# Kernel optimization log

Hardware: AMD Instinct MI355X
Metric: run time of the kernel (lower is better)

The kernel has to match this reference:

```python
import jax, jax.numpy as jnp
import numpy as np

B, N, F, H, OUT, K, L = 32, 2048, 3, 64, 128, 16, 3


def _edge_mlp(e, w1, b1, wo, bo):
    # Faithful to the given MLP.forward: layer1 -> ReLU -> output (layer2 is skipped!)
    return jax.nn.relu(e @ w1 + b1) @ wo + bo


def _dynamic_edge_conv(x, k, w1, b1, wo, bo):
    # x: [B, N, D]. kNN in feature space (self included, distance 0), per graph.
    sq = jnp.sum(x * x, axis=-1)                                   # [B, N]
    d2 = sq[:, :, None] + sq[:, None, :] - 2.0 * jnp.einsum('bnd,bmd->bnm', x, x)
    _, idx = jax.lax.top_k(-d2, k)                                 # [B, N, K]
    x_j = jax.vmap(lambda xb, ib: xb[ib])(x, idx)                  # [B, N, K, D] gather
    x_i = jnp.broadcast_to(x[:, :, None, :], x_j.shape)
    e = jnp.concatenate([x_i, x_j - x_i], axis=-1)                 # EdgeConv message [B,N,K,2D]
    h = _edge_mlp(e, w1, b1, wo, bo)                               # [B, N, K, H]
    return jnp.mean(h, axis=2)                                     # aggr='mean' -> [B, N, H]


def setup_inputs() -> dict:
    key = jax.random.key(0)
    ks = jax.random.split(key, 20)
    inp = {'x': jax.random.normal(ks[0], (B, N, F), dtype=jnp.float32)}
    kit = iter(ks[1:])
    for i in range(L):
        din = 2 * F if i == 0 else 2 * H
        inp[f'w1_{i}'] = jax.random.normal(next(kit), (din, H), jnp.float32) / np.sqrt(din)
        inp[f'b1_{i}'] = jnp.zeros((H,), jnp.float32)
        inp[f'wo_{i}'] = jax.random.normal(next(kit), (H, H), jnp.float32) / np.sqrt(H)
        inp[f'bo_{i}'] = jnp.zeros((H,), jnp.float32)
    inp['fw1'] = jax.random.normal(next(kit), (H, H), jnp.float32) / np.sqrt(H)
    inp['fb1'] = jnp.zeros((H,), jnp.float32)
    inp['fw2'] = jax.random.normal(next(kit), (H, OUT), jnp.float32) / np.sqrt(H)
    inp['fb2'] = jnp.zeros((OUT,), jnp.float32)
    return inp


def reference(x, w1_0, b1_0, wo_0, bo_0, w1_1, b1_1, wo_1, bo_1, w1_2, b1_2, wo_2, bo_2, fw1, fb1, fw2, fb2):
    layers = [(w1_0, b1_0, wo_0, bo_0), (w1_1, b1_1, wo_1, bo_1), (w1_2, b1_2, wo_2, bo_2)]
    h = x
    for (w1, b1, wo, bo) in layers:
        h = _dynamic_edge_conv(h, K, w1, b1, wo, bo)
    g = jnp.mean(h, axis=1)                                        # global_mean_pool -> [B, H]
    return jax.nn.relu(g @ fw1 + fb1) @ fw2 + fb2                  # [B, OUT]
```

## Files before the change

kernel.cpp:

```cpp
#include <hip/hip_runtime.h>

#define BB 32
#define NN 2048
#define FF 3
#define HH 64
#define OUTC 128
#define KK 16
#define BN (BB * NN)

typedef __attribute__((ext_vector_type(8))) __bf16 bf16x8;
typedef __attribute__((ext_vector_type(4))) float f32x4;

__device__ __forceinline__ unsigned int packkey(float d2, unsigned int m) {
    unsigned int bb = __builtin_bit_cast(unsigned int, d2);
    unsigned int msk = (unsigned int)((int)bb >> 31);
    unsigned int srt = bb ^ (msk | 0x80000000u);
    return (srt & 0xFFFFF800u) | m;
}

__device__ __forceinline__ unsigned long long pack64(float d2, unsigned int j) {
    unsigned int bb = __builtin_bit_cast(unsigned int, d2);
    unsigned int msk = (unsigned int)((int)bb >> 31);
    unsigned int srt = bb ^ (msk | 0x80000000u);
    return ((unsigned long long)srt << 11) | j;
}

__device__ __forceinline__ void ce(unsigned int& a, unsigned int& b) {
    unsigned int lo = a < b ? a : b;
    unsigned int hi = a < b ? b : a;
    a = lo; b = hi;
}

__device__ __forceinline__ void sort16(unsigned int k[16]) {
#pragma unroll
    for (int p = 1; p < 16; p <<= 1)
#pragma unroll
        for (int q = p; q >= 1; q >>= 1)
#pragma unroll
            for (int j = q % p; j + q < 16; j += 2 * q)
#pragma unroll
                for (int i = 0; i < q; ++i) {
                    int x = i + j, y = i + j + q;
                    if (y < 16 && (x / (2 * p) == y / (2 * p))) ce(k[x], k[y]);
                }
}

__device__ __forceinline__ void merge16(unsigned int keys[16], const unsigned int nk[16]) {
    unsigned int t[16];
#pragma unroll
    for (int i = 0; i < 16; ++i) {
        unsigned int b = nk[15 - i];
        t[i] = keys[i] < b ? keys[i] : b;
    }
#pragma unroll
    for (int d = 8; d >= 1; d >>= 1)
#pragma unroll
        for (int i = 0; i < 16; ++i)
            if ((i & d) == 0) ce(t[i], t[i ^ d]);
#pragma unroll
    for (int i = 0; i < 16; ++i) keys[i] = t[i];
}

__global__ __launch_bounds__(256) void prep3_kernel(const float* __restrict__ x,
                                                    const float* __restrict__ w1,
                                                    const float* __restrict__ b1,
                                                    float* __restrict__ sqo,
                                                    float* __restrict__ P,
                                                    float* __restrict__ Q) {
    const int tid = threadIdx.x;
    const int h = tid & 63;
    const int pl = tid >> 6;
    const long p = (long)blockIdx.x * 4 + pl;
    const float* fp = x + p * 3;
    const float f0 = fp[0], f1 = fp[1], f2 = fp[2];
    if (h == 0) sqo[p] = f0 * f0 + f1 * f1 + f2 * f2;
    float accp = 0.f, accq = 0.f;
    const float fv[3] = {f0, f1, f2};
#pragma unroll
    for (int d = 0; d < 3; ++d) {
        float wa = w1[d * HH + h];
        float wb = w1[(3 + d) * HH + h];
        accp = fmaf(fv[d], wa - wb, accp);
        accq = fmaf(fv[d], wb, accq);
    }
    P[p * HH + h] = accp + b1[h];
    Q[p * HH + h] = accq;
}

__global__ __launch_bounds__(256) void prep64_kernel(const float* __restrict__ feat,
                                                     const float* __restrict__ w1,
                                                     const float* __restrict__ b1,
                                                     __bf16* __restrict__ fbf,
                                                     float* __restrict__ sqo,
                                                     float* __restrict__ P,
                                                     float* __restrict__ Q) {
    __shared__ float rows[64 * HH];
    const int tid = threadIdx.x;
    const int h = tid & 63;
    const int wv = tid >> 6;
    const long row0 = (long)blockIdx.x * 64;

    float wdiff[64], wbv[64];
#pragma unroll
    for (int d = 0; d < 64; ++d) {
        float wa = w1[d * HH + h];
        float wb_ = w1[(HH + d) * HH + h];
        wdiff[d] = wa - wb_;
        wbv[d] = wb_;
    }
    const float bv = b1[h];

    {
        const float4* src = (const float4*)(feat + row0 * HH);
        float4* dst = (float4*)rows;
#pragma unroll
        for (int i = 0; i < 4; ++i) dst[tid + 256 * i] = src[tid + 256 * i];
    }
    __syncthreads();

    for (int r = wv * 16; r < wv * 16 + 16; ++r) {
        const long p = row0 + r;
        float fvh = rows[r * HH + h];
        fbf[p * HH + h] = (__bf16)fvh;
        float s = fvh * fvh;
        s += __shfl_xor(s, 1);
        s += __shfl_xor(s, 2);
        s += __shfl_xor(s, 4);
        s += __shfl_xor(s, 8);
        s += __shfl_xor(s, 16);
        s += __shfl_xor(s, 32);
        if (h == 0) sqo[p] = s;

        float ap0 = 0.f, ap1 = 0.f, aq0 = 0.f, aq1 = 0.f;
#pragma unroll
        for (int d4 = 0; d4 < 16; ++d4) {
            float4 fv = *(const float4*)&rows[r * HH + d4 * 4];
            ap0 = fmaf(fv.x, wdiff[4 * d4 + 0], ap0);
            aq0 = fmaf(fv.x, wbv[4 * d4 + 0], aq0);
            ap1 = fmaf(fv.y, wdiff[4 * d4 + 1], ap1);
            aq1 = fmaf(fv.y, wbv[4 * d4 + 1], aq1);
            ap0 = fmaf(fv.z, wdiff[4 * d4 + 2], ap0);
            aq0 = fmaf(fv.z, wbv[4 * d4 + 2], aq0);
            ap1 = fmaf(fv.w, wdiff[4 * d4 + 3], ap1);
            aq1 = fmaf(fv.w, wbv[4 * d4 + 3], aq1);
        }
        P[p * HH + h] = (ap0 + ap1) + bv;
        Q[p * HH + h] = aq0 + aq1;
    }
}

__global__ __launch_bounds__(256) void knn3_filter_kernel(const float* __restrict__ x,
                                                          const float* __restrict__ sq,
                                                          unsigned short* __restrict__ idx32) {
    __shared__ float4 lds_c[256];
    __shared__ unsigned int Km[64 * 68];
    const int tid = threadIdx.x;
    const int xcd = blockIdx.x & 7;
    const int ii = blockIdx.x >> 3;
    const int b = xcd + 8 * (ii >> 5);
    const int rg = ii & 31;
    const long pbase = (long)b * NN;
    const int r = tid >> 2, slot = tid & 3;
    const int row = rg * 64 + r;

    const float* rp = x + (pbase + row) * 3;
    const float xr0 = rp[0], xr1 = rp[1], xr2 = rp[2];

    unsigned int keys[KK];
#pragma unroll
    for (int j = 0; j < KK; ++j) keys[j] = 0xFFFFFFFFu;

    float c0, c1, c2, c3;
    {
        const float* cp = x + (pbase + tid) * 3;
        c0 = cp[0]; c1 = cp[1]; c2 = cp[2]; c3 = sq[pbase + tid];
    }

    for (int t = 0; t < NN / 256; ++t) {
        __syncthreads();
        lds_c[tid] = make_float4(c0, c1, c2, c3);
        __syncthreads();
        if (t < NN / 256 - 1) {
            const int m = (t + 1) * 256 + tid;
            const float* cp = x + (pbase + m) * 3;
            c0 = cp[0]; c1 = cp[1]; c2 = cp[2]; c3 = sq[pbase + m];
        }
#pragma unroll
        for (int bb = 0; bb < 4; ++bb) {
            unsigned int nk[16];
#pragma unroll
            for (int cc = 0; cc < 16; ++cc) {
                const int li = bb * 64 + cc * 4 + slot;
                float4 v = lds_c[li];
                float dot = fmaf(xr0, v.x, fmaf(xr1, v.y, xr2 * v.z));
                float d2 = fmaf(-2.0f, dot, v.w);
                nk[cc] = packkey(d2, (unsigned int)(t * 256 + li));
            }
            sort16(nk);
            merge16(keys, nk);
        }
    }

    {
        uint4* kw = (uint4*)&Km[r * 68 + slot * 16];
#pragma unroll
        for (int q = 0; q < 4; ++q)
            kw[q] = make_uint4(keys[4 * q], keys[4 * q + 1], keys[4 * q + 2], keys[4 * q + 3]);
    }
    __syncthreads();
    if (slot < 2) {
        const unsigned int* k0 = &Km[r * 68 + slot * 32];
        const unsigned int* k1 = k0 + 16;
        unsigned short ms[16];
#pragma unroll
        for (int j = 0; j < 16; ++j) {
            unsigned int a = k0[j], bv = k1[15 - j];
            ms[j] = (unsigned short)((a < bv ? a : bv) & 0x7FFu);
        }
        uint4* op = (uint4*)(idx32 + ((pbase + row) * 32 + slot * 16));
        op[0] = ((const uint4*)ms)[0];
        op[1] = ((const uint4*)ms)[1];
    }
}

#define APAD 72
#define DPAD 68

__global__ __launch_bounds__(256) void knn_filter_kernel(const __bf16* __restrict__ fbf,
                                                         const float* __restrict__ sq,
                                                         unsigned short* __restrict__ idx32) {
    __shared__ __align__(16) unsigned char smem[2 * 64 * APAD * 2];
    __shared__ __align__(16) float SqD[2 * 64];

    const int tid = threadIdx.x;
    const int xcd = blockIdx.x & 7;
    const int ii = blockIdx.x >> 3;
    const int b = xcd + 8 * (ii >> 5);
    const int rg = ii & 31;
    const long pbase = (long)b * NN;
    const int row0 = rg * 64;
    const int ci = tid >> 2, ch = tid & 3;
    const int wv = tid >> 6, ln = tid & 63;
    const int n16 = ln & 15, quad = ln >> 4;

    bf16x8 rf0, rf1;
    {
        const __bf16* rp = fbf + (pbase + row0 + wv * 16 + n16) * 64 + quad * 8;
        rf0 = *(const bf16x8*)rp;
        rf1 = *(const bf16x8*)(rp + 32);
    }

    unsigned int keys[KK];
#pragma unroll
    for (int j = 0; j < KK; ++j) keys[j] = 0xFFFFFFFFu;

    uint4 pv0, pv1;
    float psq;
    {
        const __bf16* src = fbf + (pbase + ci) * 64 + ch * 16;
        pv0 = *(const uint4*)src;
        pv1 = *(const uint4*)(src + 8);
        psq = (tid < 64) ? sq[pbase + tid] : 0.f;
    }
    {
        __bf16* B0 = (__bf16*)smem;
        *(uint4*)&B0[ci * APAD + ch * 16] = pv0;
        *(uint4*)&B0[ci * APAD + ch * 16 + 8] = pv1;
        if (tid < 64) SqD[tid] = psq;
    }
    __syncthreads();

    for (int t = 0; t < NN / 64; ++t) {
        const int cur = t & 1;
        const __bf16* Bc = (const __bf16*)smem + cur * 64 * APAD;
        const float* Sc = SqD + cur * 64;

        if (t < NN / 64 - 1) {
            const __bf16* src = fbf + (pbase + (long)(t + 1) * 64 + ci) * 64 + ch * 16;
            pv0 = *(const uint4*)src;
            pv1 = *(const uint4*)(src + 8);
            if (tid < 64) psq = sq[pbase + (t + 1) * 64 + tid];
        }

        unsigned int nk[16];
#pragma unroll
        for (int ct = 0; ct < 4; ++ct) {
            const __bf16* cp = &Bc[(ct * 16 + n16) * APAD + quad * 8];
            bf16x8 cf0 = *(const bf16x8*)cp;
            bf16x8 cf1 = *(const bf16x8*)(cp + 32);
            f32x4 acc = {0.f, 0.f, 0.f, 0.f};
            acc = __builtin_amdgcn_mfma_f32_16x16x32_bf16(cf0, rf0, acc, 0, 0, 0);
            acc = __builtin_amdgcn_mfma_f32_16x16x32_bf16(cf1, rf1, acc, 0, 0, 0);
            f32x4 sv = *(const f32x4*)&Sc[ct * 16 + quad * 4];
            const unsigned int mb = (unsigned int)(t * 64 + ct * 16 + quad * 4);
#pragma unroll
            for (int rr = 0; rr < 4; ++rr)
                nk[ct * 4 + rr] = packkey(fmaf(-2.0f, acc[rr], sv[rr]), mb + rr);
        }

        if (t < NN / 64 - 1) {
            __bf16* Bn = (__bf16*)smem + (cur ^ 1) * 64 * APAD;
            *(uint4*)&Bn[ci * APAD + ch * 16] = pv0;
            *(uint4*)&Bn[ci * APAD + ch * 16 + 8] = pv1;
            if (tid < 64) SqD[(cur ^ 1) * 64 + tid] = psq;
        }

        sort16(nk);
        merge16(keys, nk);

        __syncthreads();
    }

    unsigned int* stg = (unsigned int*)smem;
    {
        uint4* kw = (uint4*)&stg[(wv * 16 + n16) * DPAD + quad * 16];
#pragma unroll
        for (int q = 0; q < 4; ++q)
            kw[q] = make_uint4(keys[4 * q], keys[4 * q + 1], keys[4 * q + 2], keys[4 * q + 3]);
    }
    __syncthreads();
    const int r = tid >> 2, slot = tid & 3;
    if (slot < 2) {
        const unsigned int* k0 = &stg[r * DPAD + slot * 32];
        const unsigned int* k1 = k0 + 16;
        unsigned short ms[16];
#pragma unroll
        for (int j = 0; j < 16; ++j) {
            unsigned int a = k0[j], bv = k1[15 - j];
            ms[j] = (unsigned short)((a < bv ? a : bv) & 0x7FFu);
        }
        uint4* op = (uint4*)(idx32 + ((pbase + row0 + r) * 32 + slot * 16));
        op[0] = ((const uint4*)ms)[0];
        op[1] = ((const uint4*)ms)[1];
    }
}

template <int D>
__global__ __launch_bounds__(256) void rescore_gather_kernel(const float* __restrict__ feat,
                                                             const float* __restrict__ sq,
                                                             const unsigned short* __restrict__ idx32,
                                                             const float* __restrict__ P,
                                                             const float* __restrict__ Q,
                                                             const float* __restrict__ wo,
                                                             const float* __restrict__ bo,
                                                             float* __restrict__ outf) {
    __shared__ unsigned long long ScK[4][2][32];
    __shared__ int Li[4][2][KK];
    __shared__ float Rl[4][2][HH];

    const int tid = threadIdx.x;
    const int wv = tid >> 6, ln = tid & 63;
    const int rw = ln >> 5, c = ln & 31;
    const int xcd = blockIdx.x & 7;
    const int ii = blockIdx.x >> 3;
    const int batch = xcd + 8 * (ii >> 8);
    const int rb = ii & 255;
    const long pbase = (long)batch * NN;
    const long pblk = pbase + (long)rb * 8;
    const int rA = wv * 2;
    const long prow = pblk + rA + rw;

    const int jown = (int)idx32[prow * 32 + c];
    const float sqown = sq[pbase + jown];

    if constexpr (D == 64) {
        const int cg = ln >> 2, e = ln & 3;
#pragma unroll
        for (int rr = 0; rr < 2; ++rr) {
            const float* rbase = feat + (pblk + rA + rr) * 64;
            const float4 rv0 = *(const float4*)(rbase + 0 * 16 + e * 4);
            const float4 rv1 = *(const float4*)(rbase + 1 * 16 + e * 4);
            const float4 rv2 = *(const float4*)(rbase + 2 * 16 + e * 4);
            const float4 rv3 = *(const float4*)(rbase + 3 * 16 + e * 4);
#pragma unroll
            for (int pp = 0; pp < 2; ++pp) {
                const int srcl = rr * 32 + pp * 16 + cg;
                const int jq = __shfl(jown, srcl);
                const float sqc = __shfl(sqown, srcl);
                const float* cb = feat + (pbase + jq) * 64;
                const float4 cv0 = *(const float4*)(cb + 0 * 16 + e * 4);
                const float4 cv1 = *(const float4*)(cb + 1 * 16 + e * 4);
                const float4 cv2 = *(const float4*)(cb + 2 * 16 + e * 4);
                const float4 cv3 = *(const float4*)(cb + 3 * 16 + e * 4);
                float part = 0.f;
                part = fmaf(rv0.x, cv0.x, part); part = fmaf(rv0.y, cv0.y, part);
                part = fmaf(rv0.z, cv0.z, part); part = fmaf(rv0.w, cv0.w, part);
                part = fmaf(rv1.x, cv1.x, part); part = fmaf(rv1.y, cv1.y, part);
                part = fmaf(rv1.z, cv1.z, part); part = fmaf(rv1.w, cv1.w, part);
                part = fmaf(rv2.x, cv2.x, part); part = fmaf(rv2.y, cv2.y, part);
                part = fmaf(rv2.z, cv2.z, part); part = fmaf(rv2.w, cv2.w, part);
                part = fmaf(rv3.x, cv3.x, part); part = fmaf(rv3.y, cv3.y, part);
                part = fmaf(rv3.z, cv3.z, part); part = fmaf(rv3.w, cv3.w, part);
                part += __shfl_xor(part, 1);
                part += __shfl_xor(part, 2);
                if (e == 0)
                    ScK[wv][rr][pp * 16 + cg] =
                        pack64(fmaf(-2.0f, part, sqc), (unsigned int)jq);
            }
        }
    } else {
        const float* rp = feat + prow * 3;
        const float xr0 = rp[0], xr1 = rp[1], xr2 = rp[2];
        const float* cp = feat + (pbase + jown) * 3;
        const float dot = fmaf(xr0, cp[0], fmaf(xr1, cp[1], xr2 * cp[2]));
        ScK[wv][rw][c] = pack64(fmaf(-2.0f, dot, sqown), (unsigned int)jown);
    }
    asm volatile("s_waitcnt lgkmcnt(0)" ::: "memory");
    __builtin_amdgcn_sched_barrier(0);

    {
        const unsigned long long mykey = ScK[wv][rw][c];
        int rank = 0;
#pragma unroll
        for (int m = 0; m < 32; ++m)
            rank += (ScK[wv][rw][m] < mykey) ? 1 : 0;
        if (rank < KK) Li[wv][rw][rank] = (int)(mykey & 0x7FFu);
    }
    asm volatile("s_waitcnt lgkmcnt(0)" ::: "memory");
    __builtin_amdgcn_sched_barrier(0);

    const int h = ln;
    const long pA = pblk + rA;
    const float PvA = P[pA * HH + h];
    const float PvB = P[(pA + 1) * HH + h];
    float accA = 0.f, accB = 0.f;
#pragma unroll
    for (int kq = 0; kq < 4; ++kq) {
        const int4 a4 = *(const int4*)&Li[wv][0][kq * 4];
        const int4 b4 = *(const int4*)&Li[wv][1][kq * 4];
        accA += fmaxf(PvA + Q[(pbase + a4.x) * HH + h], 0.f);
        accA += fmaxf(PvA + Q[(pbase + a4.y) * HH + h], 0.f);
        accA += fmaxf(PvA + Q[(pbase + a4.z) * HH + h], 0.f);
        accA += fmaxf(PvA + Q[(pbase + a4.w) * HH + h], 0.f);
        accB += fmaxf(PvB + Q[(pbase + b4.x) * HH + h], 0.f);
        accB += fmaxf(PvB + Q[(pbase + b4.y) * HH + h], 0.f);
        accB += fmaxf(PvB + Q[(pbase + b4.z) * HH + h], 0.f);
        accB += fmaxf(PvB + Q[(pbase + b4.w) * HH + h], 0.f);
    }
    Rl[wv][0][h] = accA * (1.f / KK);
    Rl[wv][1][h] = accB * (1.f / KK);
    asm volatile("s_waitcnt lgkmcnt(0)" ::: "memory");
    __builtin_amdgcn_sched_barrier(0);

    float oA = bo[h];
    float oB = oA;
#pragma unroll
    for (int l4 = 0; l4 < 16; ++l4) {
        const float4 ra = *(const float4*)&Rl[wv][0][l4 * 4];
        const float4 rb4 = *(const float4*)&Rl[wv][1][l4 * 4];
        const float* wp = wo + (l4 * 4) * HH + h;
        const float w0 = wp[0], w1 = wp[HH], w2 = wp[2 * HH], w3 = wp[3 * HH];
        oA = fmaf(ra.x, w0, oA);  oB = fmaf(rb4.x, w0, oB);
        oA = fmaf(ra.y, w1, oA);  oB = fmaf(rb4.y, w1, oB);
        oA = fmaf(ra.z, w2, oA);  oB = fmaf(rb4.z, w2, oB);
        oA = fmaf(ra.w, w3, oA);  oB = fmaf(rb4.w, w3, oB);
    }
    outf[pA * HH + h] = oA;
    outf[(pA + 1) * HH + h] = oB;
}

__global__ __launch_bounds__(256) void pool_partial_kernel(const float* __restrict__ feat,
                                                           float* __restrict__ pp) {
    __shared__ float part[4][HH];
    const int batch = blockIdx.x >> 3;
    const int chk = blockIdx.x & 7;
    const int tid = threadIdx.x;
    const int h = tid & 63;
    const int sub = tid >> 6;
    float s = 0.f;
    const float* fp = feat + ((long)batch * NN + chk * 256 + sub * 64) * HH + h;
    for (int n = 0; n < 64; ++n) s += fp[(long)n * HH];
    part[sub][h] = s;
    __syncthreads();
    if (tid < HH)
        pp[(batch * 8 + chk) * HH + h] = part[0][h] + part[1][h] + part[2][h] + part[3][h];
}

__global__ __launch_bounds__(256) void head_kernel(const float* __restrict__ pp,
                                                   const float* __restrict__ fw1,
                                                   const float* __restrict__ fb1,
                                                   const float* __restrict__ fw2,
                                                   const float* __restrict__ fb2,
                                                   float* __restrict__ out) {
    __shared__ float g[HH];
    __shared__ float tl[HH];
    const int b = blockIdx.x;
    const int tid = threadIdx.x;
    if (tid < HH) {
        float s = 0.f;
#pragma unroll
        for (int c = 0; c < 8; ++c) s += pp[(b * 8 + c) * HH + tid];
        g[tid] = s * (1.f / NN);
    }
    __syncthreads();
    if (tid < HH) {
        float a = fb1[tid];
#pragma unroll
        for (int l = 0; l < HH; ++l) a = fmaf(g[l], fw1[l * HH + tid], a);
        tl[tid] = fmaxf(a, 0.f);
    }
    __syncthreads();
    if (tid < OUTC) {
        float o = fb2[tid];
#pragma unroll
        for (int l = 0; l < HH; ++l) o = fmaf(tl[l], fw2[l * OUTC + tid], o);
        out[(long)b * OUTC + tid] = o;
    }
}

extern "C" void kernel_launch(void* const* d_in, const int* in_sizes, int n_in,
                              void* d_out, int out_size, void* d_ws, size_t ws_size,
                              hipStream_t stream) {
    const float* x    = (const float*)d_in[0];
    const float* w1_0 = (const float*)d_in[1];
    const float* b1_0 = (const float*)d_in[2];
    const float* wo_0 = (const float*)d_in[3];
    const float* bo_0 = (const float*)d_in[4];
    const float* w1_1 = (const float*)d_in[5];
    const float* b1_1 = (const float*)d_in[6];
    const float* wo_1 = (const float*)d_in[7];
    const float* bo_1 = (const float*)d_in[8];
    const float* w1_2 = (const float*)d_in[9];
    const float* b1_2 = (const float*)d_in[10];
    const float* wo_2 = (const float*)d_in[11];
    const float* bo_2 = (const float*)d_in[12];
    const float* fw1  = (const float*)d_in[13];
    const float* fb1  = (const float*)d_in[14];
    const float* fw2  = (const float*)d_in[15];
    const float* fb2  = (const float*)d_in[16];
    float* out = (float*)d_out;

    float* featA = (float*)d_ws;
    float* featB = featA + (long)BN * HH;
    float* Pb    = featB + (long)BN * HH;
    float* Qb    = Pb + (long)BN * HH;
    float* sqb   = Qb + (long)BN * HH;
    unsigned short* idx32 = (unsigned short*)(sqb + BN);
    float* ppb   = (float*)(idx32 + (long)BN * 32);

    __bf16* fbf1 = (__bf16*)featB;
    __bf16* fbf2 = (__bf16*)featA;

    prep3_kernel<<<BN / 4, 256, 0, stream>>>(x, w1_0, b1_0, sqb, Pb, Qb);
    knn3_filter_kernel<<<BB * 32, 256, 0, stream>>>(x, sqb, idx32);
    rescore_gather_kernel<3><<<BN / 8, 256, 0, stream>>>(x, sqb, idx32, Pb, Qb, wo_0, bo_0, featA);

    prep64_kernel<<<BN / 64, 256, 0, stream>>>(featA, w1_1, b1_1, fbf1, sqb, Pb, Qb);
    knn_filter_kernel<<<BB * 32, 256, 0, stream>>>(fbf1, sqb, idx32);
    rescore_gather_kernel<64><<<BN / 8, 256, 0, stream>>>(featA, sqb, idx32, Pb, Qb, wo_1, bo_1, featB);

    prep64_kernel<<<BN / 64, 256, 0, stream>>>(featB, w1_2, b1_2, fbf2, sqb, Pb, Qb);
    knn_filter_kernel<<<BB * 32, 256, 0, stream>>>(fbf2, sqb, idx32);
    rescore_gather_kernel<64><<<BN / 8, 256, 0, stream>>>(featB, sqb, idx32, Pb, Qb, wo_2, bo_2, featA);

    pool_partial_kernel<<<BB * 8, 256, 0, stream>>>(featA, ppb);
    head_kernel<<<BB, 256, 0, stream>>>(ppb, fw1, fb1, fw2, fb2, out);
}
```

Before: 524.7 us.

## Drop LDS staging in kNN filter kernels, read candidates directly from global/L2

Both kNN filter kernels stop staging candidate tiles through double-buffered shared memory with block-wide barriers. Each thread now loads candidate features and squared norms straight from global memory, relying on L1/L2 caching. For the 3-D layer, prep3 writes a packed float4 (x,y,z,|x|^2) array so each candidate is one vector load. The final cross-thread merge swaps __syncthreads for a wave-local lgkmcnt wait, and launch bounds now request 4 blocks per CU. This removes barrier stalls and LDS traffic but adds redundant global loads per wave. The barrier replacement is only safe if every row's keys in Km are written and read by the same wave.

```diff
diff --git a/kernel.cpp b/kernel.cpp
--- a/kernel.cpp
+++ b/kernel.cpp
@@ -66,14 +66,19 @@
                                                     const float* __restrict__ b1,
                                                     float* __restrict__ sqo,
                                                     float* __restrict__ P,
-                                                    float* __restrict__ Q) {
+                                                    float* __restrict__ Q,
+                                                    float* __restrict__ x4) {
     const int tid = threadIdx.x;
     const int h = tid & 63;
     const int pl = tid >> 6;
     const long p = (long)blockIdx.x * 4 + pl;
     const float* fp = x + p * 3;
     const float f0 = fp[0], f1 = fp[1], f2 = fp[2];
-    if (h == 0) sqo[p] = f0 * f0 + f1 * f1 + f2 * f2;
+    if (h == 0) {
+        const float s = f0 * f0 + f1 * f1 + f2 * f2;
+        sqo[p] = s;
+        *(float4*)(x4 + p * 4) = make_float4(f0, f1, f2, s);
+    }
     float accp = 0.f, accq = 0.f;
     const float fv[3] = {f0, f1, f2};
 #pragma unroll
@@ -149,10 +154,8 @@
     }
 }
 
-__global__ __launch_bounds__(256) void knn3_filter_kernel(const float* __restrict__ x,
-                                                          const float* __restrict__ sq,
-                                                          unsigned short* __restrict__ idx32) {
-    __shared__ float4 lds_c[256];
+__global__ __launch_bounds__(256, 4) void knn3_filter_kernel(const float* __restrict__ x4,
+                                                             unsigned short* __restrict__ idx32) {
     __shared__ unsigned int Km[64 * 68];
     const int tid = threadIdx.x;
     const int xcd = blockIdx.x & 7;
@@ -163,37 +166,24 @@
     const int r = tid >> 2, slot = tid & 3;
     const int row = rg * 64 + r;
 
-    const float* rp = x + (pbase + row) * 3;
-    const float xr0 = rp[0], xr1 = rp[1], xr2 = rp[2];
+    const f32x4 xr = *(const f32x4*)(x4 + (pbase + row) * 4);
+    const float xr0 = xr[0], xr1 = xr[1], xr2 = xr[2];
 
     unsigned int keys[KK];
 #pragma unroll
     for (int j = 0; j < KK; ++j) keys[j] = 0xFFFFFFFFu;
 
-    float c0, c1, c2, c3;
-    {
-        const float* cp = x + (pbase + tid) * 3;
-        c0 = cp[0]; c1 = cp[1]; c2 = cp[2]; c3 = sq[pbase + tid];
-    }
-
+#pragma unroll 1
     for (int t = 0; t < NN / 256; ++t) {
-        __syncthreads();
-        lds_c[tid] = make_float4(c0, c1, c2, c3);
-        __syncthreads();
-        if (t < NN / 256 - 1) {
-            const int m = (t + 1) * 256 + tid;
-            const float* cp = x + (pbase + m) * 3;
-            c0 = cp[0]; c1 = cp[1]; c2 = cp[2]; c3 = sq[pbase + m];
-        }
 #pragma unroll
         for (int bb = 0; bb < 4; ++bb) {
             unsigned int nk[16];
 #pragma unroll
             for (int cc = 0; cc < 16; ++cc) {
                 const int li = bb * 64 + cc * 4 + slot;
-                float4 v = lds_c[li];
-                float dot = fmaf(xr0, v.x, fmaf(xr1, v.y, xr2 * v.z));
-                float d2 = fmaf(-2.0f, dot, v.w);
+                const f32x4 v = *(const f32x4*)(x4 + (pbase + t * 256 + li) * 4);
+                float dot = fmaf(xr0, v[0], fmaf(xr1, v[1], xr2 * v[2]));
+                float d2 = fmaf(-2.0f, dot, v[3]);
                 nk[cc] = packkey(d2, (unsigned int)(t * 256 + li));
             }
             sort16(nk);
@@ -207,7 +197,8 @@
         for (int q = 0; q < 4; ++q)
             kw[q] = make_uint4(keys[4 * q], keys[4 * q + 1], keys[4 * q + 2], keys[4 * q + 3]);
     }
-    __syncthreads();
+    asm volatile("s_waitcnt lgkmcnt(0)" ::: "memory");
+    __builtin_amdgcn_sched_barrier(0);
     if (slot < 2) {
         const unsigned int* k0 = &Km[r * 68 + slot * 32];
         const unsigned int* k1 = k0 + 16;
@@ -223,14 +214,12 @@
     }
 }
 
-#define APAD 72
 #define DPAD 68
 
-__global__ __launch_bounds__(256) void knn_filter_kernel(const __bf16* __restrict__ fbf,
-                                                         const float* __restrict__ sq,
-                                                         unsigned short* __restrict__ idx32) {
-    __shared__ __align__(16) unsigned char smem[2 * 64 * APAD * 2];
-    __shared__ __align__(16) float SqD[2 * 64];
+__global__ __launch_bounds__(256, 4) void knn_filter_kernel(const __bf16* __restrict__ fbf,
+                                                            const float* __restrict__ sq,
+                                                            unsigned short* __restrict__ idx32) {
+    __shared__ unsigned int Km[64 * DPAD];
 
     const int tid = threadIdx.x;
     const int xcd = blockIdx.x & 7;
@@ -239,7 +228,6 @@
     const int rg = ii & 31;
     const long pbase = (long)b * NN;
     const int row0 = rg * 64;
-    const int ci = tid >> 2, ch = tid & 3;
     const int wv = tid >> 6, ln = tid & 63;
     const int n16 = ln & 15, quad = ln >> 4;
 
@@ -254,74 +242,38 @@
 #pragma unroll
     for (int j = 0; j < KK; ++j) keys[j] = 0xFFFFFFFFu;
 
-    uint4 pv0, pv1;
-    float psq;
-    {
-        const __bf16* src = fbf + (pbase + ci) * 64 + ch * 16;
-        pv0 = *(const uint4*)src;
-        pv1 = *(const uint4*)(src + 8);
-        psq = (tid < 64) ? sq[pbase + tid] : 0.f;
-    }
-    {
-        __bf16* B0 = (__bf16*)smem;
-        *(uint4*)&B0[ci * APAD + ch * 16] = pv0;
-        *(uint4*)&B0[ci * APAD + ch * 16 + 8] = pv1;
-        if (tid < 64) SqD[tid] = psq;
-    }
-    __syncthreads();
-
+#pragma unroll 1
     for (int t = 0; t < NN / 64; ++t) {
-        const int cur = t & 1;
-        const __bf16* Bc = (const __bf16*)smem + cur * 64 * APAD;
-        const float* Sc = SqD + cur * 64;
-
-        if (t < NN / 64 - 1) {
-            const __bf16* src = fbf + (pbase + (long)(t + 1) * 64 + ci) * 64 + ch * 16;
-            pv0 = *(const uint4*)src;
-            pv1 = *(const uint4*)(src + 8);
-            if (tid < 64) psq = sq[pbase + (t + 1) * 64 + tid];
-        }
-
         unsigned int nk[16];
 #pragma unroll
         for (int ct = 0; ct < 4; ++ct) {
-            const __bf16* cp = &Bc[(ct * 16 + n16) * APAD + quad * 8];
+            const __bf16* cp = fbf + (pbase + t * 64 + ct * 16 + n16) * 64 + quad * 8;
             bf16x8 cf0 = *(const bf16x8*)cp;
             bf16x8 cf1 = *(const bf16x8*)(cp + 32);
             f32x4 acc = {0.f, 0.f, 0.f, 0.f};
             acc = __builtin_amdgcn_mfma_f32_16x16x32_bf16(cf0, rf0, acc, 0, 0, 0);
             acc = __builtin_amdgcn_mfma_f32_16x16x32_bf16(cf1, rf1, acc, 0, 0, 0);
-            f32x4 sv = *(const f32x4*)&Sc[ct * 16 + quad * 4];
+            const f32x4 sv = *(const f32x4*)(sq + pbase + t * 64 + ct * 16 + quad * 4);
             const unsigned int mb = (unsigned int)(t * 64 + ct * 16 + quad * 4);
 #pragma unroll
             for (int rr = 0; rr < 4; ++rr)
                 nk[ct * 4 + rr] = packkey(fmaf(-2.0f, acc[rr], sv[rr]), mb + rr);
         }
-
-        if (t < NN / 64 - 1) {
-            __bf16* Bn = (__bf16*)smem + (cur ^ 1) * 64 * APAD;
-            *(uint4*)&Bn[ci * APAD + ch * 16] = pv0;
-            *(uint4*)&Bn[ci * APAD + ch * 16 + 8] = pv1;
-            if (tid < 64) SqD[(cur ^ 1) * 64 + tid] = psq;
-        }
-
         sort16(nk);
         merge16(keys, nk);
-
-        __syncthreads();
-    }
-
-    unsigned int* stg = (unsigned int*)smem;
+    }
+
     {
-        uint4* kw = (uint4*)&stg[(wv * 16 + n16) * DPAD + quad * 16];
+        uint4* kw = (uint4*)&Km[(wv * 16 + n16) * DPAD + quad * 16];
 #pragma unroll
         for (int q = 0; q < 4; ++q)
             kw[q] = make_uint4(keys[4 * q], keys[4 * q + 1], keys[4 * q + 2], keys[4 * q + 3]);
     }
-    __syncthreads();
+    asm volatile("s_waitcnt lgkmcnt(0)" ::: "memory");
+    __builtin_amdgcn_sched_barrier(0);
     const int r = tid >> 2, slot = tid & 3;
     if (slot < 2) {
-        const unsigned int* k0 = &stg[r * DPAD + slot * 32];
+        const unsigned int* k0 = &Km[r * DPAD + slot * 32];
         const unsigned int* k1 = k0 + 16;
         unsigned short ms[16];
 #pragma unroll
@@ -537,12 +489,13 @@
     float* sqb   = Qb + (long)BN * HH;
     unsigned short* idx32 = (unsigned short*)(sqb + BN);
     float* ppb   = (float*)(idx32 + (long)BN * 32);
+    float* x4b   = ppb + 32 * 8 * HH;
 
     __bf16* fbf1 = (__bf16*)featB;
     __bf16* fbf2 = (__bf16*)featA;
 
-    prep3_kernel<<<BN / 4, 256, 0, stream>>>(x, w1_0, b1_0, sqb, Pb, Qb);
-    knn3_filter_kernel<<<BB * 32, 256, 0, stream>>>(x, sqb, idx32);
+    prep3_kernel<<<BN / 4, 256, 0, stream>>>(x, w1_0, b1_0, sqb, Pb, Qb, x4b);
+    knn3_filter_kernel<<<BB * 32, 256, 0, stream>>>(x4b, idx32);
     rescore_gather_kernel<3><<<BN / 8, 256, 0, stream>>>(x, sqb, idx32, Pb, Qb, wo_0, bo_0, featA);
 
     prep64_kernel<<<BN / 64, 256, 0, stream>>>(featA, w1_1, b1_1, fbf1, sqb, Pb, Qb);
```

Measured after the change: 679.3 us. +29.5%, slower.

## Load kNN candidate tiles straight into registers, dropping LDS staging and barriers

Applied to the files above, without the earlier changes.

The kNN filter kernel no longer stages each 64-candidate tile through double-buffered LDS guarded by __syncthreads. Each wave now loads its MFMA candidate fragments and squared norms directly from global memory into a two-deep register buffer, so the distance, sort and merge work runs without block-wide barriers. The final key staging keeps only a small LDS array and uses a wave-local waitcnt instead of a block barrier, which is valid because each wave reads back only its own rows. In exchange every wave fetches the whole candidate set separately, raising L2 and global traffic, and the register double buffer raises VGPR use. The launch bounds are also tightened to target four blocks per CU.

```diff
diff --git a/kernel.cpp b/kernel.cpp
--- a/kernel.cpp
+++ b/kernel.cpp
@@ -223,14 +223,39 @@
     }
 }
 
-#define APAD 72
 #define DPAD 68
 
-__global__ __launch_bounds__(256) void knn_filter_kernel(const __bf16* __restrict__ fbf,
-                                                         const float* __restrict__ sq,
-                                                         unsigned short* __restrict__ idx32) {
-    __shared__ __align__(16) unsigned char smem[2 * 64 * APAD * 2];
-    __shared__ __align__(16) float SqD[2 * 64];
+__device__ __forceinline__ void load_tile(bf16x8 (&dst)[8], const __bf16* __restrict__ p) {
+#pragma unroll
+    for (int ct = 0; ct < 4; ++ct) {
+        dst[2 * ct]     = *(const bf16x8*)(p + ct * 16 * 64);
+        dst[2 * ct + 1] = *(const bf16x8*)(p + ct * 16 * 64 + 32);
+    }
+}
+
+__device__ __forceinline__ void compute_tile(const bf16x8 (&cf)[8], bf16x8 rf0, bf16x8 rf1,
+                                             const float* __restrict__ sqp, int tbase, int quad,
+                                             unsigned int keys[16]) {
+    unsigned int nk[16];
+#pragma unroll
+    for (int ct = 0; ct < 4; ++ct) {
+        f32x4 acc = {0.f, 0.f, 0.f, 0.f};
+        acc = __builtin_amdgcn_mfma_f32_16x16x32_bf16(cf[2 * ct], rf0, acc, 0, 0, 0);
+        acc = __builtin_amdgcn_mfma_f32_16x16x32_bf16(cf[2 * ct + 1], rf1, acc, 0, 0, 0);
+        const f32x4 sv = *(const f32x4*)(sqp + ct * 16 + quad * 4);
+        const unsigned int mb = (unsigned int)(tbase + ct * 16 + quad * 4);
+#pragma unroll
+        for (int rr = 0; rr < 4; ++rr)
+            nk[ct * 4 + rr] = packkey(fmaf(-2.0f, acc[rr], sv[rr]), mb + rr);
+    }
+    sort16(nk);
+    merge16(keys, nk);
+}
+
+__global__ __launch_bounds__(256, 4) void knn_filter_kernel(const __bf16* __restrict__ fbf,
+                                                            const float* __restrict__ sq,
+                                                            unsigned short* __restrict__ idx32) {
+    __shared__ unsigned int Km[64 * DPAD];
 
     const int tid = threadIdx.x;
     const int xcd = blockIdx.x & 7;
@@ -239,7 +264,6 @@
     const int rg = ii & 31;
     const long pbase = (long)b * NN;
     const int row0 = rg * 64;
-    const int ci = tid >> 2, ch = tid & 3;
     const int wv = tid >> 6, ln = tid & 63;
     const int n16 = ln & 15, quad = ln >> 4;
 
@@ -254,74 +278,31 @@
 #pragma unroll
     for (int j = 0; j < KK; ++j) keys[j] = 0xFFFFFFFFu;
 
-    uint4 pv0, pv1;
-    float psq;
+    const __bf16* cb0 = fbf + (pbase + n16) * 64 + quad * 8;
+    const float* sqb_ = sq + pbase;
+
+    bf16x8 ca[8], cbuf[8];
+    load_tile(ca, cb0);
+#pragma unroll 1
+    for (int i = 0; i < 16; ++i) {
+        load_tile(cbuf, cb0 + (long)(2 * i + 1) * 4096);
+        compute_tile(ca, rf0, rf1, sqb_ + (2 * i) * 64, (2 * i) * 64, quad, keys);
+        if (i < 15)
+            load_tile(ca, cb0 + (long)(2 * i + 2) * 4096);
+        compute_tile(cbuf, rf0, rf1, sqb_ + (2 * i + 1) * 64, (2 * i + 1) * 64, quad, keys);
+    }
+
     {
-        const __bf16* src = fbf + (pbase + ci) * 64 + ch * 16;
-        pv0 = *(const uint4*)src;
-        pv1 = *(const uint4*)(src + 8);
-        psq = (tid < 64) ? sq[pbase + tid] : 0.f;
-    }
-    {
-        __bf16* B0 = (__bf16*)smem;
-        *(uint4*)&B0[ci * APAD + ch * 16] = pv0;
-        *(uint4*)&B0[ci * APAD + ch * 16 + 8] = pv1;
-        if (tid < 64) SqD[tid] = psq;
-    }
-    __syncthreads();
-
-    for (int t = 0; t < NN / 64; ++t) {
-        const int cur = t & 1;
-        const __bf16* Bc = (const __bf16*)smem + cur * 64 * APAD;
-        const float* Sc = SqD + cur * 64;
-
-        if (t < NN / 64 - 1) {
-            const __bf16* src = fbf + (pbase + (long)(t + 1) * 64 + ci) * 64 + ch * 16;
-            pv0 = *(const uint4*)src;
-            pv1 = *(const uint4*)(src + 8);
-            if (tid < 64) psq = sq[pbase + (t + 1) * 64 + tid];
-        }
-
-        unsigned int nk[16];
-#pragma unroll
-        for (int ct = 0; ct < 4; ++ct) {
-            const __bf16* cp = &Bc[(ct * 16 + n16) * APAD + quad * 8];
-            bf16x8 cf0 = *(const bf16x8*)cp;
-            bf16x8 cf1 = *(const bf16x8*)(cp + 32);
-            f32x4 acc = {0.f, 0.f, 0.f, 0.f};
-            acc = __builtin_amdgcn_mfma_f32_16x16x32_bf16(cf0, rf0, acc, 0, 0, 0);
-            acc = __builtin_amdgcn_mfma_f32_16x16x32_bf16(cf1, rf1, acc, 0, 0, 0);
-            f32x4 sv = *(const f32x4*)&Sc[ct * 16 + quad * 4];
-            const unsigned int mb = (unsigned int)(t * 64 + ct * 16 + quad * 4);
-#pragma unroll
-            for (int rr = 0; rr < 4; ++rr)
-                nk[ct * 4 + rr] = packkey(fmaf(-2.0f, acc[rr], sv[rr]), mb + rr);
-        }
-
-        if (t < NN / 64 - 1) {
-            __bf16* Bn = (__bf16*)smem + (cur ^ 1) * 64 * APAD;
-            *(uint4*)&Bn[ci * APAD + ch * 16] = pv0;
-            *(uint4*)&Bn[ci * APAD + ch * 16 + 8] = pv1;
-            if (tid < 64) SqD[(cur ^ 1) * 64 + tid] = psq;
-        }
-
-        sort16(nk);
-        merge16(keys, nk);
-
-        __syncthreads();
-    }
-
-    unsigned int* stg = (unsigned int*)smem;
-    {
-        uint4* kw = (uint4*)&stg[(wv * 16 + n16) * DPAD + quad * 16];
+        uint4* kw = (uint4*)&Km[(wv * 16 + n16) * DPAD + quad * 16];
 #pragma unroll
         for (int q = 0; q < 4; ++q)
             kw[q] = make_uint4(keys[4 * q], keys[4 * q + 1], keys[4 * q + 2], keys[4 * q + 3]);
     }
-    __syncthreads();
+    asm volatile("s_waitcnt lgkmcnt(0)" ::: "memory");
+    __builtin_amdgcn_sched_barrier(0);
     const int r = tid >> 2, slot = tid & 3;
     if (slot < 2) {
-        const unsigned int* k0 = &stg[r * DPAD + slot * 32];
+        const unsigned int* k0 = &Km[r * DPAD + slot * 32];
         const unsigned int* k1 = k0 + 16;
         unsigned short ms[16];
 #pragma unroll
```

After: 667.0 us. +27.1%, slower.

## Split kNN candidate range across two blocks per row group

Applied to the files above, without the earlier changes.

Each kNN filter kernel now launches twice as many blocks, and each block scans only half of the 2048 candidates. Within a block, the per-slot top-16 lists are merged down to a single top-16, and each half writes its own 16 indices into the 32-slot candidate buffer. Before, one block produced 32 candidates (two merged halves) from the full range; now the two halves come from disjoint candidate ranges. This doubles grid parallelism (1024 to 2048 blocks) and halves the serial loop length, at the cost of more merge work per row in a single thread (slot 0).

```diff
diff --git a/kernel.cpp b/kernel.cpp
--- a/kernel.cpp
+++ b/kernel.cpp
@@ -59,6 +59,15 @@
             if ((i & d) == 0) ce(t[i], t[i ^ d]);
 #pragma unroll
     for (int i = 0; i < 16; ++i) keys[i] = t[i];
+}
+
+__device__ __forceinline__ void load16(unsigned int dst[16], const unsigned int* __restrict__ src) {
+#pragma unroll
+    for (int q = 0; q < 4; ++q) {
+        uint4 v = ((const uint4*)src)[q];
+        dst[4 * q] = v.x; dst[4 * q + 1] = v.y;
+        dst[4 * q + 2] = v.z; dst[4 * q + 3] = v.w;
+    }
 }
 
 __global__ __launch_bounds__(256) void prep3_kernel(const float* __restrict__ x,
@@ -157,8 +166,11 @@
     const int tid = threadIdx.x;
     const int xcd = blockIdx.x & 7;
     const int ii = blockIdx.x >> 3;
-    const int b = xcd + 8 * (ii >> 5);
-    const int rg = ii & 31;
+    const int b = xcd + 8 * (ii >> 6);
+    const int sub = ii & 63;
+    const int rg = sub >> 1;
+    const int half = sub & 1;
+    const int cbase0 = half * 1024;
     const long pbase = (long)b * NN;
     const int r = tid >> 2, slot = tid & 3;
     const int row = rg * 64 + r;
@@ -172,16 +184,16 @@
 
     float c0, c1, c2, c3;
     {
-        const float* cp = x + (pbase + tid) * 3;
-        c0 = cp[0]; c1 = cp[1]; c2 = cp[2]; c3 = sq[pbase + tid];
-    }
-
-    for (int t = 0; t < NN / 256; ++t) {
+        const float* cp = x + (pbase + cbase0 + tid) * 3;
+        c0 = cp[0]; c1 = cp[1]; c2 = cp[2]; c3 = sq[pbase + cbase0 + tid];
+    }
+
+    for (int t = 0; t < 4; ++t) {
         __syncthreads();
         lds_c[tid] = make_float4(c0, c1, c2, c3);
         __syncthreads();
-        if (t < NN / 256 - 1) {
-            const int m = (t + 1) * 256 + tid;
+        if (t < 3) {
+            const int m = cbase0 + (t + 1) * 256 + tid;
             const float* cp = x + (pbase + m) * 3;
             c0 = cp[0]; c1 = cp[1]; c2 = cp[2]; c3 = sq[pbase + m];
         }
@@ -194,7 +206,7 @@
                 float4 v = lds_c[li];
                 float dot = fmaf(xr0, v.x, fmaf(xr1, v.y, xr2 * v.z));
                 float d2 = fmaf(-2.0f, dot, v.w);
-                nk[cc] = packkey(d2, (unsigned int)(t * 256 + li));
+                nk[cc] = packkey(d2, (unsigned int)(cbase0 + t * 256 + li));
             }
             sort16(nk);
             merge16(keys, nk);
@@ -208,16 +220,19 @@
             kw[q] = make_uint4(keys[4 * q], keys[4 * q + 1], keys[4 * q + 2], keys[4 * q + 3]);
     }
     __syncthreads();
-    if (slot < 2) {
-        const unsigned int* k0 = &Km[r * 68 + slot * 32];
-        const unsigned int* k1 = k0 + 16;
+    if (slot == 0) {
+        unsigned int m1[16], m2[16], tmp[16];
+        load16(m1, &Km[r * 68]);
+        load16(tmp, &Km[r * 68 + 16]);
+        merge16(m1, tmp);
+        load16(m2, &Km[r * 68 + 32]);
+        load16(tmp, &Km[r * 68 + 48]);
+        merge16(m2, tmp);
+        merge16(m1, m2);
         unsigned short ms[16];
 #pragma unroll
-        for (int j = 0; j < 16; ++j) {
-            unsigned int a = k0[j], bv = k1[15 - j];
-            ms[j] = (unsigned short)((a < bv ? a : bv) & 0x7FFu);
-        }
-        uint4* op = (uint4*)(idx32 + ((pbase + row) * 32 + slot * 16));
+        for (int j = 0; j < 16; ++j) ms[j] = (unsigned short)(m1[j] & 0x7FFu);
+        uint4* op = (uint4*)(idx32 + ((pbase + row) * 32 + half * 16));
         op[0] = ((const uint4*)ms)[0];
         op[1] = ((const uint4*)ms)[1];
     }
@@ -235,8 +250,11 @@
     const int tid = threadIdx.x;
     const int xcd = blockIdx.x & 7;
     const int ii = blockIdx.x >> 3;
-    const int b = xcd + 8 * (ii >> 5);
-    const int rg = ii & 31;
+    const int b = xcd + 8 * (ii >> 6);
+    const int sub = ii & 63;
+    const int rg = sub >> 1;
+    const int half = sub & 1;
+    const int cbase0 = half * 1024;
     const long pbase = (long)b * NN;
     const int row0 = rg * 64;
     const int ci = tid >> 2, ch = tid & 3;
@@ -257,10 +275,10 @@
     uint4 pv0, pv1;
     float psq;
     {
-        const __bf16* src = fbf + (pbase + ci) * 64 + ch * 16;
+        const __bf16* src = fbf + (pbase + cbase0 + ci) * 64 + ch * 16;
         pv0 = *(const uint4*)src;
         pv1 = *(const uint4*)(src + 8);
-        psq = (tid < 64) ? sq[pbase + tid] : 0.f;
+        psq = (tid < 64) ? sq[pbase + cbase0 + tid] : 0.f;
     }
     {
         __bf16* B0 = (__bf16*)smem;
@@ -270,16 +288,16 @@
     }
     __syncthreads();
 
-    for (int t = 0; t < NN / 64; ++t) {
+    for (int t = 0; t < 16; ++t) {
         const int cur = t & 1;
         const __bf16* Bc = (const __bf16*)smem + cur * 64 * APAD;
         const float* Sc = SqD + cur * 64;
 
-        if (t < NN / 64 - 1) {
-            const __bf16* src = fbf + (pbase + (long)(t + 1) * 64 + ci) * 64 + ch * 16;
+        if (t < 15) {
+            const __bf16* src = fbf + (pbase + cbase0 + (long)(t + 1) * 64 + ci) * 64 + ch * 16;
             pv0 = *(const uint4*)src;
             pv1 = *(const uint4*)(src + 8);
-            if (tid < 64) psq = sq[pbase + (t + 1) * 64 + tid];
+            if (tid < 64) psq = sq[pbase + cbase0 + (t + 1) * 64 + tid];
         }
 
         unsigned int nk[16];
@@ -292,13 +310,13 @@
             acc = __builtin_amdgcn_mfma_f32_16x16x32_bf16(cf0, rf0, acc, 0, 0, 0);
             acc = __builtin_amdgcn_mfma_f32_16x16x32_bf16(cf1, rf1, acc, 0, 0, 0);
             f32x4 sv = *(const f32x4*)&Sc[ct * 16 + quad * 4];
-            const unsigned int mb = (unsigned int)(t * 64 + ct * 16 + quad * 4);
+            const unsigned int mb = (unsigned int)(cbase0 + t * 64 + ct * 16 + quad * 4);
 #pragma unroll
             for (int rr = 0; rr < 4; ++rr)
                 nk[ct * 4 + rr] = packkey(fmaf(-2.0f, acc[rr], sv[rr]), mb + rr);
         }
 
-        if (t < NN / 64 - 1) {
+        if (t < 15) {
             __bf16* Bn = (__bf16*)smem + (cur ^ 1) * 64 * APAD;
             *(uint4*)&Bn[ci * APAD + ch * 16] = pv0;
             *(uint4*)&Bn[ci * APAD + ch * 16 + 8] = pv1;
@@ -320,16 +338,19 @@
     }
     __syncthreads();
     const int r = tid >> 2, slot = tid & 3;
-    if (slot < 2) {
-        const unsigned int* k0 = &stg[r * DPAD + slot * 32];
-        const unsigned int* k1 = k0 + 16;
+    if (slot == 0) {
+        unsigned int m1[16], m2[16], tmp[16];
+        load16(m1, &stg[r * DPAD]);
+        load16(tmp, &stg[r * DPAD + 16]);
+        merge16(m1, tmp);
+        load16(m2, &stg[r * DPAD + 32]);
+        load16(tmp, &stg[r * DPAD + 48]);
+        merge16(m2, tmp);
+        merge16(m1, m2);
         unsigned short ms[16];
 #pragma unroll
-        for (int j = 0; j < 16; ++j) {
-            unsigned int a = k0[j], bv = k1[15 - j];
-            ms[j] = (unsigned short)((a < bv ? a : bv) & 0x7FFu);
-        }
-        uint4* op = (uint4*)(idx32 + ((pbase + row0 + r) * 32 + slot * 16));
+        for (int j = 0; j < 16; ++j) ms[j] = (unsigned short)(m1[j] & 0x7FFu);
+        uint4* op = (uint4*)(idx32 + ((pbase + row0 + r) * 32 + half * 16));
         op[0] = ((const uint4*)ms)[0];
         op[1] = ((const uint4*)ms)[1];
     }
@@ -542,15 +563,15 @@
     __bf16* fbf2 = (__bf16*)featA;
 
     prep3_kernel<<<BN / 4, 256, 0, stream>>>(x, w1_0, b1_0, sqb, Pb, Qb);
-    knn3_filter_kernel<<<BB * 32, 256, 0, stream>>>(x, sqb, idx32);
+    knn3_filter_kernel<<<BB * 64, 256, 0, stream>>>(x, sqb, idx32);
     rescore_gather_kernel<3><<<BN / 8, 256, 0, stream>>>(x, sqb, idx32, Pb, Qb, wo_0, bo_0, featA);
 
     prep64_kernel<<<BN / 64, 256, 0, stream>>>(featA, w1_1, b1_1, fbf1, sqb, Pb, Qb);
-    knn_filter_kernel<<<BB * 32, 256, 0, stream>>>(fbf1, sqb, idx32);
+    knn_filter_kernel<<<BB * 64, 256, 0, stream>>>(fbf1, sqb, idx32);
     rescore_gather_kernel<64><<<BN / 8, 256, 0, stream>>>(featA, sqb, idx32, Pb, Qb, wo_1, bo_1, featB);
 
     prep64_kernel<<<BN / 64, 256, 0, stream>>>(featB, w1_2, b1_2, fbf2, sqb, Pb, Qb);
-    knn_filter_kernel<<<BB * 32, 256, 0, stream>>>(fbf2, sqb, idx32);
+    knn_filter_kernel<<<BB * 64, 256, 0, stream>>>(fbf2, sqb, idx32);
     rescore_gather_kernel<64><<<BN / 8, 256, 0, stream>>>(featB, sqb, idx32, Pb, Qb, wo_2, bo_2, featA);
 
     pool_partial_kernel<<<BB * 8, 256, 0, stream>>>(featA, ppb);
```

Measured after the change: 522.8 us. About the same (-0.4%).
